# Kernel tuning notes

Hardware: AMD Instinct MI355X
Metric: run time of the kernel (lower is better)

The kernel has to match this reference:

```python
import jax, jax.numpy as jnp
import numpy as np

NEG_SLOPE = 0.2  # PyG GATv2Conv default
TOPK = 10        # hard-coded in original forward


def setup_inputs() -> dict:
    key = jax.random.key(0)
    N, E, D, L = 50000, 640000, 128, 3
    ks = jax.random.split(key, 12)
    s = 1.0 / np.sqrt(D)
    x = jax.random.normal(ks[0], (N, D), jnp.float32)
    edge_index = jax.random.randint(ks[1], (2, E), 0, N, dtype=jnp.int64)
    edge_attributes = jax.random.normal(ks[2], (E, D), jnp.float32)
    # GATv2 per-layer params (heads=1): lin_l (src), lin_r (dst), lin_edge, att, out bias
    Wl = jax.random.normal(ks[3], (L, D, D), jnp.float32) * s
    bl = jnp.zeros((L, D), jnp.float32)
    Wr = jax.random.normal(ks[4], (L, D, D), jnp.float32) * s
    br = jnp.zeros((L, D), jnp.float32)
    We = jax.random.normal(ks[5], (L, D, D), jnp.float32) * s
    att = jax.random.normal(ks[6], (L, D), jnp.float32) * s
    bias = jnp.zeros((L, D), jnp.float32)
    # final Conv1d(D, 1, 1) == linear projection D -> 1 per node
    Wf = jax.random.normal(ks[7], (D, 1), jnp.float32) * s
    bf = jnp.zeros((1,), jnp.float32)
    return {"x": x, "edge_index": edge_index, "edge_attributes": edge_attributes,
            "Wl": Wl, "bl": bl, "Wr": Wr, "br": br, "We": We, "att": att,
            "bias": bias, "Wf": Wf, "bf": bf}


def _gatv2_layer(x, src, dst, ea, N, Wl, bl, Wr, br, We, att, bias):
    xl = x @ Wl + bl            # [N, D] source transform
    xr = x @ Wr + br            # [N, D] target transform
    ee = ea @ We                # [E', D] edge transform (no bias in PyG lin_edge)
    m = jax.nn.leaky_relu(xl[src] + xr[dst] + ee, NEG_SLOPE)  # [E', D]
    logits = m @ att            # [E']
    # per-destination softmax (every node has a self-loop -> no empty segments)
    mx = jax.ops.segment_max(logits, dst, num_segments=N)
    w = jnp.exp(logits - mx[dst])
    den = jax.ops.segment_sum(w, dst, num_segments=N)
    alpha = w / den[dst]
    out = jax.ops.segment_sum(xl[src] * alpha[:, None], dst, num_segments=N)
    return out + bias


def reference(x, edge_index, edge_attributes, Wl, bl, Wr, br, We, att, bias, Wf, bf):
    N, D = x.shape
    src, dst = edge_index[0], edge_index[1]
    loop = jnp.arange(N, dtype=src.dtype)
    # add_self_loops with fill_value='mean': loop attr = mean of incoming edge attrs
    cnt = jax.ops.segment_sum(jnp.ones_like(dst, dtype=x.dtype), dst, num_segments=N)
    loop_attr = jax.ops.segment_sum(edge_attributes, dst, num_segments=N) / jnp.maximum(cnt, 1.0)[:, None]
    src_f = jnp.concatenate([src, loop])
    dst_f = jnp.concatenate([dst, loop])
    ea = jnp.concatenate([edge_attributes, loop_attr], axis=0)
    L = Wl.shape[0]
    for i in range(L):
        x = _gatv2_layer(x, src_f, dst_f, ea, N, Wl[i], bl[i], Wr[i], br[i], We[i], att[i], bias[i])
    scores = (x @ Wf)[:, 0] + bf[0]   # Conv1d(D,1,1): per-node scalar score [N]
    vals, idx = jax.lax.top_k(scores, TOPK)
    return vals, idx
```

## Files before the change

### kernel.cpp

```cpp
#include <hip/hip_runtime.h>
#include <hip/hip_bf16.h>
#include <float.h>

#define DD 128
#define NEG_SLOPE 0.2f

typedef __attribute__((ext_vector_type(8))) short bf16x8;
typedef __attribute__((ext_vector_type(4))) float f32x4;

__device__ __forceinline__ float lrelu(float v) {
    return fmaxf(v, 0.0f) + NEG_SLOPE * fminf(v, 0.0f);
}

__device__ __forceinline__ unsigned short f2bf(float f) {
    unsigned u = __float_as_uint(f);
    u += 0x7fff + ((u >> 16) & 1);
    return (unsigned short)(u >> 16);
}
__device__ __forceinline__ float bf2f(unsigned short h) {
    return __uint_as_float(((unsigned)h) << 16);
}


__global__ void k_hist(const int* __restrict__ dst, int E, int* __restrict__ cnt) {
    int i = blockIdx.x * blockDim.x + threadIdx.x;
    if (i < E) atomicAdd(&cnt[dst[i]], 1);
}

__global__ __launch_bounds__(1024) void k_scan(const int* __restrict__ cnt,
                                               int* __restrict__ row_ptr, int N) {
    __shared__ int sums[1024];
    int tid = threadIdx.x;
    int total = N + 1;
    int chunk = (total + 1023) / 1024;
    int lo = tid * chunk;
    int hi = min(lo + chunk, total);
    int s = 0;
    for (int i = lo; i < hi; ++i) s += (i < N) ? (cnt[i] + 1) : 0;
    sums[tid] = s;
    __syncthreads();
    for (int off = 1; off < 1024; off <<= 1) {
        int t = (tid >= off) ? sums[tid - off] : 0;
        __syncthreads();
        sums[tid] += t;
        __syncthreads();
    }
    int run = sums[tid] - s;
    for (int i = lo; i < hi; ++i) {
        row_ptr[i] = run;
        run += (i < N) ? (cnt[i] + 1) : 0;
    }
}

__global__ void k_scatter(const int* __restrict__ dst, int E, int N,
                          const int* __restrict__ row_ptr, int* __restrict__ fill,
                          const int* __restrict__ cnt, int* __restrict__ eids) {
    int i = blockIdx.x * blockDim.x + threadIdx.x;
    int tot = E + N;
    if (i >= tot) return;
    if (i < E) {
        int d = dst[i];
        int p = atomicAdd(&fill[d], 1);
        eids[row_ptr[d] + p] = i;
    } else {
        int n = i - E;
        eids[row_ptr[n] + cnt[n]] = E + n;
    }
}

__global__ void k_sort_rows(const int* __restrict__ row_ptr, int* __restrict__ eids, int N) {
    int n = blockIdx.x * blockDim.x + threadIdx.x;
    if (n >= N) return;
    int s = row_ptr[n], e = row_ptr[n + 1];
    for (int i = s + 1; i < e; ++i) {
        int v = eids[i];
        int j = i - 1;
        while (j >= s && eids[j] > v) { eids[j + 1] = eids[j]; --j; }
        eids[j + 1] = v;
    }
}

__global__ void k_invert(const int* __restrict__ eids, const int* __restrict__ srcArr,
                         int* __restrict__ pos, int* __restrict__ csr_src, int Etot, int E) {
    int p = blockIdx.x * blockDim.x + threadIdx.x;
    if (p >= Etot) return;
    int eid = eids[p];
    pos[eid] = p;
    csr_src[p] = (eid < E) ? srcArr[eid] : (eid - E);
}

__global__ __launch_bounds__(256) void k_loop_attr(const float* __restrict__ ea,
                                                   const int* __restrict__ row_ptr,
                                                   const int* __restrict__ cnt,
                                                   const int* __restrict__ eids,
                                                   float* __restrict__ loop_attr, int N) {
    int wid = (blockIdx.x * blockDim.x + threadIdx.x) >> 6;
    int lane = threadIdx.x & 63;
    if (wid >= N) return;
    int s = row_ptr[wid];
    int c = cnt[wid];
    float2 acc = make_float2(0.f, 0.f);
    for (int c0 = 0; c0 < c; c0 += 64) {
        int m = min(64, c - c0);
        int eid = 0;
        if (lane < m) eid = eids[s + c0 + lane];
        int p = 0;
        for (; p + 4 <= m; p += 4) {
            int e0 = __shfl(eid, p), e1 = __shfl(eid, p + 1);
            int e2 = __shfl(eid, p + 2), e3 = __shfl(eid, p + 3);
            float2 v0 = *reinterpret_cast<const float2*>(ea + (size_t)e0 * DD + 2 * lane);
            float2 v1 = *reinterpret_cast<const float2*>(ea + (size_t)e1 * DD + 2 * lane);
            float2 v2 = *reinterpret_cast<const float2*>(ea + (size_t)e2 * DD + 2 * lane);
            float2 v3 = *reinterpret_cast<const float2*>(ea + (size_t)e3 * DD + 2 * lane);
            acc.x += v0.x; acc.y += v0.y;
            acc.x += v1.x; acc.y += v1.y;
            acc.x += v2.x; acc.y += v2.y;
            acc.x += v3.x; acc.y += v3.y;
        }
        for (; p < m; ++p) {
            int e = __shfl(eid, p);
            float2 v = *reinterpret_cast<const float2*>(ea + (size_t)e * DD + 2 * lane);
            acc.x += v.x; acc.y += v.y;
        }
    }
    float inv = 1.0f / fmaxf((float)c, 1.0f);
    float2 o = make_float2(acc.x * inv, acc.y * inv);
    *reinterpret_cast<float2*>(loop_attr + (size_t)wid * DD + 2 * lane) = o;
}

__global__ void k_prepack(const float* __restrict__ W, unsigned short* __restrict__ WA, int L) {
    int idx = blockIdx.x * blockDim.x + threadIdx.x;
    int total = L * DD * DD;
    if (idx >= total) return;
    int l = idx >> 14;
    int rem = idx & 16383;
    int k = rem >> 7;
    int j = rem & 127;
    float w = W[(size_t)l * 16384 + (size_t)k * DD + j];
    unsigned short h = f2bf(w);
    unsigned short lo = f2bf(w - bf2f(h));
    int ks = k >> 5, g = (k >> 3) & 3, i = k & 7;
    size_t off = ((size_t)(ks * 4 + g) * DD + j) * 8 + i;
    unsigned short* base = WA + (size_t)l * 32768;
    base[off] = h;
    base[16384 + off] = lo;
}


__global__ __launch_bounds__(512, 2) void k_gemm_mfma(
    const float* __restrict__ X, const unsigned short* __restrict__ WA,
    const float* __restrict__ b, float* __restrict__ Y, int N) {

    __shared__ unsigned short WAs[32768];
    {
        const uint4* gsrc = reinterpret_cast<const uint4*>(WA);
        uint4* ldst = reinterpret_cast<uint4*>(WAs);
        int t = threadIdx.x;
        #pragma unroll
        for (int i = 0; i < 8; ++i) ldst[t + i * 512] = gsrc[t + i * 512];
    }
    __syncthreads();

    int tid  = threadIdx.x;
    int lane = tid & 63;
    int wv   = tid >> 6;
    int lc   = lane & 15;
    int g    = lane >> 4;

    int r0 = blockIdx.x * 256 + wv * 32;
    int rv[2]; bool ok[2];
    const float* rp[2];
    #pragma unroll
    for (int nf = 0; nf < 2; ++nf) {
        rv[nf] = r0 + nf * 16 + lc;
        ok[nf] = (rv[nf] < N);
        rp[nf] = X + (size_t)(ok[nf] ? rv[nf] : 0) * DD;
    }

    f32x4 acc[8][2];
    #pragma unroll
    for (int m = 0; m < 8; ++m)
        #pragma unroll
        for (int n = 0; n < 2; ++n)
            acc[m][n] = (f32x4){0.f, 0.f, 0.f, 0.f};

    float4 pr0[2], pr1[2];
    #pragma unroll
    for (int nf = 0; nf < 2; ++nf) {
        pr0[nf] = *reinterpret_cast<const float4*>(rp[nf] + g * 8);
        pr1[nf] = *reinterpret_cast<const float4*>(rp[nf] + g * 8 + 4);
    }

    #pragma unroll
    for (int ks = 0; ks < 4; ++ks) {
        bf16x8 Bh[2], Bl[2];
        #pragma unroll
        for (int nf = 0; nf < 2; ++nf) {
            float v[8] = {pr0[nf].x, pr0[nf].y, pr0[nf].z, pr0[nf].w,
                          pr1[nf].x, pr1[nf].y, pr1[nf].z, pr1[nf].w};
            #pragma unroll
            for (int i = 0; i < 8; ++i) {
                unsigned short h = f2bf(v[i]);
                Bh[nf][i] = (short)h;
                Bl[nf][i] = (short)f2bf(v[i] - bf2f(h));
            }
        }
        if (ks < 3) {
            int k0n = (ks + 1) * 32 + g * 8;
            #pragma unroll
            for (int nf = 0; nf < 2; ++nf) {
                pr0[nf] = *reinterpret_cast<const float4*>(rp[nf] + k0n);
                pr1[nf] = *reinterpret_cast<const float4*>(rp[nf] + k0n + 4);
            }
        }
        #pragma unroll
        for (int mf = 0; mf < 8; ++mf) {
            int aoff = ((ks * 4 + g) * DD + (mf * 16 + lc)) * 8;
            bf16x8 Ah = *reinterpret_cast<const bf16x8*>(&WAs[aoff]);
            bf16x8 Al = *reinterpret_cast<const bf16x8*>(&WAs[16384 + aoff]);
            #pragma unroll
            for (int nf = 0; nf < 2; ++nf) {
                acc[mf][nf] = __builtin_amdgcn_mfma_f32_16x16x32_bf16(Ah, Bh[nf], acc[mf][nf], 0, 0, 0);
                acc[mf][nf] = __builtin_amdgcn_mfma_f32_16x16x32_bf16(Al, Bh[nf], acc[mf][nf], 0, 0, 0);
                acc[mf][nf] = __builtin_amdgcn_mfma_f32_16x16x32_bf16(Ah, Bl[nf], acc[mf][nf], 0, 0, 0);
            }
        }
    }

    #pragma unroll
    for (int mf = 0; mf < 8; ++mf) {
        int f0 = mf * 16 + g * 4;
        float4 bv = *reinterpret_cast<const float4*>(b + f0);
        #pragma unroll
        for (int nf = 0; nf < 2; ++nf) {
            if (!ok[nf]) continue;
            float4 o;
            o.x = acc[mf][nf][0] + bv.x;
            o.y = acc[mf][nf][1] + bv.y;
            o.z = acc[mf][nf][2] + bv.z;
            o.w = acc[mf][nf][3] + bv.w;
            *reinterpret_cast<float4*>(Y + (size_t)rv[nf] * DD + f0) = o;
        }
    }
}

__global__ __launch_bounds__(512, 2) void k_edge_mfma(
    const float* __restrict__ ea, const float* __restrict__ loop_attr,
    const int* __restrict__ srcArr, const int* __restrict__ dstArr,
    const unsigned short* __restrict__ WA, const float* __restrict__ att,
    const float* __restrict__ xl, const float* __restrict__ xr,
    const int* __restrict__ pos, float* __restrict__ wlog, int E, int Etot) {

    __shared__ unsigned short WAs[32768];
    {
        const uint4* gsrc = reinterpret_cast<const uint4*>(WA);
        uint4* ldst = reinterpret_cast<uint4*>(WAs);
        int t = threadIdx.x;
        #pragma unroll
        for (int i = 0; i < 8; ++i) ldst[t + i * 512] = gsrc[t + i * 512];
    }
    __syncthreads();

    int tid  = threadIdx.x;
    int lane = tid & 63;
    int wv   = tid >> 6;
    int lc   = lane & 15;
    int g    = lane >> 4;

    int e0 = blockIdx.x * 256 + wv * 32;

    const float* rp[2];
    int ev[2]; bool ok[2];
    #pragma unroll
    for (int nf = 0; nf < 2; ++nf) {
        int e = e0 + nf * 16 + lc;
        ev[nf] = e;
        ok[nf] = (e < Etot);
        if (e < E)         rp[nf] = ea + (size_t)e * DD;
        else if (e < Etot) rp[nf] = loop_attr + (size_t)(e - E) * DD;
        else               rp[nf] = ea;
    }

    f32x4 acc[8][2];
    #pragma unroll
    for (int m = 0; m < 8; ++m)
        #pragma unroll
        for (int n = 0; n < 2; ++n)
            acc[m][n] = (f32x4){0.f, 0.f, 0.f, 0.f};

    float4 pr0[2], pr1[2];
    #pragma unroll
    for (int nf = 0; nf < 2; ++nf) {
        pr0[nf] = *reinterpret_cast<const float4*>(rp[nf] + g * 8);
        pr1[nf] = *reinterpret_cast<const float4*>(rp[nf] + g * 8 + 4);
    }

    #pragma unroll
    for (int ks = 0; ks < 4; ++ks) {
        bf16x8 Bh[2], Bl[2];
        #pragma unroll
        for (int nf = 0; nf < 2; ++nf) {
            float v[8] = {pr0[nf].x, pr0[nf].y, pr0[nf].z, pr0[nf].w,
                          pr1[nf].x, pr1[nf].y, pr1[nf].z, pr1[nf].w};
            #pragma unroll
            for (int i = 0; i < 8; ++i) {
                unsigned short h = f2bf(v[i]);
                Bh[nf][i] = (short)h;
                Bl[nf][i] = (short)f2bf(v[i] - bf2f(h));
            }
        }
        if (ks < 3) {
            int k0n = (ks + 1) * 32 + g * 8;
            #pragma unroll
            for (int nf = 0; nf < 2; ++nf) {
                pr0[nf] = *reinterpret_cast<const float4*>(rp[nf] + k0n);
                pr1[nf] = *reinterpret_cast<const float4*>(rp[nf] + k0n + 4);
            }
        }
        #pragma unroll
        for (int mf = 0; mf < 8; ++mf) {
            int aoff = ((ks * 4 + g) * DD + (mf * 16 + lc)) * 8;
            bf16x8 Ah = *reinterpret_cast<const bf16x8*>(&WAs[aoff]);
            bf16x8 Al = *reinterpret_cast<const bf16x8*>(&WAs[16384 + aoff]);
            #pragma unroll
            for (int nf = 0; nf < 2; ++nf) {
                acc[mf][nf] = __builtin_amdgcn_mfma_f32_16x16x32_bf16(Ah, Bh[nf], acc[mf][nf], 0, 0, 0);
                acc[mf][nf] = __builtin_amdgcn_mfma_f32_16x16x32_bf16(Al, Bh[nf], acc[mf][nf], 0, 0, 0);
                acc[mf][nf] = __builtin_amdgcn_mfma_f32_16x16x32_bf16(Ah, Bl[nf], acc[mf][nf], 0, 0, 0);
            }
        }
    }

    int sn[2], dn[2];
    #pragma unroll
    for (int nf = 0; nf < 2; ++nf) {
        int e = ev[nf];
        if (e < E)       { sn[nf] = srcArr[e]; dn[nf] = dstArr[e]; }
        else if (ok[nf]) { sn[nf] = e - E; dn[nf] = e - E; }
        else             { sn[nf] = 0; dn[nf] = 0; }
    }
    float partial[2] = {0.f, 0.f};
    #pragma unroll
    for (int mf = 0; mf < 8; ++mf) {
        int f0 = mf * 16 + g * 4;
        float4 attv = *reinterpret_cast<const float4*>(att + f0);
        #pragma unroll
        for (int nf = 0; nf < 2; ++nf) {
            float4 xlv = *reinterpret_cast<const float4*>(xl + (size_t)sn[nf] * DD + f0);
            float4 xrv = *reinterpret_cast<const float4*>(xr + (size_t)dn[nf] * DD + f0);
            float t0 = acc[mf][nf][0] + xlv.x + xrv.x;
            float t1 = acc[mf][nf][1] + xlv.y + xrv.y;
            float t2 = acc[mf][nf][2] + xlv.z + xrv.z;
            float t3 = acc[mf][nf][3] + xlv.w + xrv.w;
            partial[nf] += attv.x * lrelu(t0) + attv.y * lrelu(t1)
                         + attv.z * lrelu(t2) + attv.w * lrelu(t3);
        }
    }
    #pragma unroll
    for (int nf = 0; nf < 2; ++nf) {
        float p = partial[nf];
        p += __shfl_xor(p, 16);
        p += __shfl_xor(p, 32);
        if (lane < 16 && ok[nf]) wlog[pos[ev[nf]]] = p;
    }
}

__global__ __launch_bounds__(256) void k_sfx_agg(
    const float* __restrict__ wlog, const int* __restrict__ row_ptr,
    const int* __restrict__ csr_src, const float* __restrict__ xl,
    const float* __restrict__ bias, float* __restrict__ xout, int N) {
    int wid = (blockIdx.x * blockDim.x + threadIdx.x) >> 6;
    int lane = threadIdx.x & 63;
    if (wid >= N) return;
    int s = row_ptr[wid], e = row_ptr[wid + 1];
    float mx = -FLT_MAX;
    for (int c0 = s; c0 < e; c0 += 64) {
        float l = (c0 + lane < e) ? wlog[c0 + lane] : -FLT_MAX;
        l = fmaxf(l, __shfl_xor(l, 32));
        l = fmaxf(l, __shfl_xor(l, 16));
        l = fmaxf(l, __shfl_xor(l, 8));
        l = fmaxf(l, __shfl_xor(l, 4));
        l = fmaxf(l, __shfl_xor(l, 2));
        l = fmaxf(l, __shfl_xor(l, 1));
        mx = fmaxf(mx, l);
    }
    float den = 0.f;
    for (int c0 = s; c0 < e; c0 += 64) {
        float w = (c0 + lane < e) ? __expf(wlog[c0 + lane] - mx) : 0.f;
        w += __shfl_xor(w, 32);
        w += __shfl_xor(w, 16);
        w += __shfl_xor(w, 8);
        w += __shfl_xor(w, 4);
        w += __shfl_xor(w, 2);
        w += __shfl_xor(w, 1);
        den += w;
    }
    float inv = 1.0f / den;
    float2 acc = make_float2(0.f, 0.f);
    for (int c0 = s; c0 < e; c0 += 64) {
        int m = min(64, e - c0);
        float av = 0.f; int sv = 0;
        if (lane < m) {
            av = __expf(wlog[c0 + lane] - mx) * inv;
            sv = csr_src[c0 + lane];
        }
        int p = 0;
        for (; p + 4 <= m; p += 4) {
            float a0 = __shfl(av, p),     a1 = __shfl(av, p + 1);
            float a2 = __shfl(av, p + 2), a3 = __shfl(av, p + 3);
            int   r0 = __shfl(sv, p),     r1 = __shfl(sv, p + 1);
            int   r2 = __shfl(sv, p + 2), r3 = __shfl(sv, p + 3);
            float2 v0 = *reinterpret_cast<const float2*>(xl + (size_t)r0 * DD + 2 * lane);
            float2 v1 = *reinterpret_cast<const float2*>(xl + (size_t)r1 * DD + 2 * lane);
            float2 v2 = *reinterpret_cast<const float2*>(xl + (size_t)r2 * DD + 2 * lane);
            float2 v3 = *reinterpret_cast<const float2*>(xl + (size_t)r3 * DD + 2 * lane);
            acc.x += a0 * v0.x; acc.y += a0 * v0.y;
            acc.x += a1 * v1.x; acc.y += a1 * v1.y;
            acc.x += a2 * v2.x; acc.y += a2 * v2.y;
            acc.x += a3 * v3.x; acc.y += a3 * v3.y;
        }
        for (; p < m; ++p) {
            float ap = __shfl(av, p);
            int   rw = __shfl(sv, p);
            float2 v = *reinterpret_cast<const float2*>(xl + (size_t)rw * DD + 2 * lane);
            acc.x += ap * v.x;
            acc.y += ap * v.y;
        }
    }
    float2 bv = *reinterpret_cast<const float2*>(bias + 2 * lane);
    float2 o = make_float2(acc.x + bv.x, acc.y + bv.y);
    *reinterpret_cast<float2*>(xout + (size_t)wid * DD + 2 * lane) = o;
}


__global__ __launch_bounds__(256) void k_scores(const float* __restrict__ X,
                                                const float* __restrict__ Wf,
                                                const float* __restrict__ bf,
                                                float* __restrict__ scores, int N) {
    int gid = blockIdx.x * blockDim.x + threadIdx.x;
    int node = gid >> 6;
    int lane = threadIdx.x & 63;
    if (node >= N) return;
    float2 xv = *reinterpret_cast<const float2*>(&X[(size_t)node * DD + lane * 2]);
    float2 wv = *reinterpret_cast<const float2*>(&Wf[lane * 2]);
    float p = xv.x * wv.x + xv.y * wv.y;
    p += __shfl_xor(p, 32);
    p += __shfl_xor(p, 16);
    p += __shfl_xor(p, 8);
    p += __shfl_xor(p, 4);
    p += __shfl_xor(p, 2);
    p += __shfl_xor(p, 1);
    if (lane == 0) scores[node] = p + bf[0];
}

__device__ __forceinline__ bool tk_better(float a, int ai, float b, int bi) {
    return (a > b) || (a == b && ai < bi);
}

__global__ __launch_bounds__(1024) void k_topk(const float* __restrict__ scores, int N,
                                               float* __restrict__ out) {
    __shared__ float lv[1024 * 10];
    __shared__ int li[1024 * 10];
    int t = threadIdx.x;
    float v[10]; int ix[10];
    #pragma unroll
    for (int j = 0; j < 10; ++j) { v[j] = -FLT_MAX; ix[j] = 0x7fffffff; }
    for (int i = t; i < N; i += 1024) {
        float sv = scores[i];
        if (tk_better(sv, i, v[9], ix[9])) {
            v[9] = sv; ix[9] = i;
            #pragma unroll
            for (int j = 9; j > 0; --j) {
                if (tk_better(v[j], ix[j], v[j - 1], ix[j - 1])) {
                    float tv = v[j]; v[j] = v[j - 1]; v[j - 1] = tv;
                    int ti = ix[j]; ix[j] = ix[j - 1]; ix[j - 1] = ti;
                }
            }
        }
    }
    #pragma unroll
    for (int j = 0; j < 10; ++j) { lv[t * 10 + j] = v[j]; li[t * 10 + j] = ix[j]; }
    __syncthreads();
    for (int sh = 512; sh >= 1; sh >>= 1) {
        if (t < sh) {
            float bv[10]; int bi[10];
            #pragma unroll
            for (int j = 0; j < 10; ++j) { bv[j] = lv[(t + sh) * 10 + j]; bi[j] = li[(t + sh) * 10 + j]; }
            float mv[10]; int mi[10];
            int i1 = 0, i2 = 0;
            #pragma unroll
            for (int k = 0; k < 10; ++k) {
                if (tk_better(v[i1], ix[i1], bv[i2], bi[i2])) { mv[k] = v[i1]; mi[k] = ix[i1]; ++i1; }
                else { mv[k] = bv[i2]; mi[k] = bi[i2]; ++i2; }
            }
            #pragma unroll
            for (int j = 0; j < 10; ++j) {
                v[j] = mv[j]; ix[j] = mi[j];
                lv[t * 10 + j] = v[j]; li[t * 10 + j] = ix[j];
            }
        }
        __syncthreads();
    }
    if (t == 0) {
        #pragma unroll
        for (int j = 0; j < 10; ++j) {
            out[j] = v[j];
            out[10 + j] = (float)ix[j];
        }
    }
}


static inline size_t alignup(size_t v) { return (v + 255) & ~(size_t)255; }

extern "C" void kernel_launch(void* const* d_in, const int* in_sizes, int n_in,
                              void* d_out, int out_size, void* d_ws, size_t ws_size,
                              hipStream_t stream) {
    const float* x    = (const float*)d_in[0];
    const int*   ei   = (const int*)d_in[1];
    const float* ea   = (const float*)d_in[2];
    const float* Wl   = (const float*)d_in[3];
    const float* bl   = (const float*)d_in[4];
    const float* Wr   = (const float*)d_in[5];
    const float* br   = (const float*)d_in[6];
    const float* We   = (const float*)d_in[7];
    const float* att  = (const float*)d_in[8];
    const float* bias = (const float*)d_in[9];
    const float* Wf   = (const float*)d_in[10];
    const float* bf   = (const float*)d_in[11];

    int N = in_sizes[0] / DD;
    int E = in_sizes[1] / 2;
    int L = in_sizes[3] / (DD * DD);
    int Etot = E + N;
    const int* src = ei;
    const int* dst = ei + E;

    size_t off = 0;
    char* wsb = (char*)d_ws;
    auto carve = [&](size_t bytes) -> void* { void* p = wsb + off; off += alignup(bytes); return p; };
    unsigned short* WAe = (unsigned short*)carve((size_t)L * 32768 * 2);
    unsigned short* WAl = (unsigned short*)carve((size_t)L * 32768 * 2);
    unsigned short* WAr = (unsigned short*)carve((size_t)L * 32768 * 2);
    int*   cnt       = (int*)carve((size_t)N * 4);
    int*   fill      = (int*)carve((size_t)N * 4);
    int*   row_ptr   = (int*)carve((size_t)(N + 1) * 4);
    int*   eids      = (int*)carve((size_t)Etot * 4);
    int*   pos       = (int*)carve((size_t)Etot * 4);
    int*   csr_src   = (int*)carve((size_t)Etot * 4);
    float* wlog      = (float*)carve((size_t)Etot * 4);
    float* loop_attr = (float*)carve((size_t)N * DD * 4);
    float* xl        = (float*)carve((size_t)N * DD * 4);
    float* xr        = (float*)carve((size_t)N * DD * 4);
    float* xa        = (float*)carve((size_t)N * DD * 4);
    float* xb        = (float*)carve((size_t)N * DD * 4);
    float* scoresBuf = (float*)carve((size_t)N * 4);
    (void)ws_size; (void)n_in; (void)out_size;

    hipMemsetAsync(cnt, 0, (size_t)N * 4, stream);
    hipMemsetAsync(fill, 0, (size_t)N * 4, stream);

    int ppBlocks = (L * DD * DD + 255) / 256;
    k_prepack<<<ppBlocks, 256, 0, stream>>>(We, WAe, L);
    k_prepack<<<ppBlocks, 256, 0, stream>>>(Wl, WAl, L);
    k_prepack<<<ppBlocks, 256, 0, stream>>>(Wr, WAr, L);
    k_hist<<<(E + 255) / 256, 256, 0, stream>>>(dst, E, cnt);
    k_scan<<<1, 1024, 0, stream>>>(cnt, row_ptr, N);
    k_scatter<<<(Etot + 255) / 256, 256, 0, stream>>>(dst, E, N, row_ptr, fill, cnt, eids);
    k_sort_rows<<<(N + 255) / 256, 256, 0, stream>>>(row_ptr, eids, N);
    k_invert<<<(Etot + 255) / 256, 256, 0, stream>>>(eids, src, pos, csr_src, Etot, E);
    int waveBlocks = (N * 64 + 255) / 256;
    k_loop_attr<<<waveBlocks, 256, 0, stream>>>(ea, row_ptr, cnt, eids, loop_attr, N);

    const float* xin = x;
    float* xout = xa;
    int gemmBlocks = (N + 255) / 256;
    int edgeBlocks = (Etot + 255) / 256;
    for (int l = 0; l < L; ++l) {
        k_gemm_mfma<<<gemmBlocks, 512, 0, stream>>>(xin, WAl + (size_t)l * 32768, bl + (size_t)l * DD, xl, N);
        k_gemm_mfma<<<gemmBlocks, 512, 0, stream>>>(xin, WAr + (size_t)l * 32768, br + (size_t)l * DD, xr, N);
        k_edge_mfma<<<edgeBlocks, 512, 0, stream>>>(ea, loop_attr, src, dst,
                                                    WAe + (size_t)l * 32768, att + (size_t)l * DD,
                                                    xl, xr, pos, wlog, E, Etot);
        k_sfx_agg<<<waveBlocks, 256, 0, stream>>>(wlog, row_ptr, csr_src, xl,
                                                  bias + (size_t)l * DD, xout, N);
        xin = xout;
        xout = (xout == xa) ? xb : xa;
    }
    k_scores<<<(N + 3) / 4, 256, 0, stream>>>(xin, Wf, bf, scoresBuf, N);
    k_topk<<<1, 1024, 0, stream>>>(scoresBuf, N, (float*)d_out);
}
```

Baseline: 1.205 ms.

## Split top-k into multi-block candidate pass and single-block final merge

Replaces the single 1024-thread top-k kernel with a two-stage reduction: 128 blocks each compute a local top-10 over a strided slice of scores, then a 64-thread kernel merges the 1280 candidates. This spreads the scan of the 50k scores over many compute units instead of one, and shortens the shared-memory merge tree. It adds one kernel launch and a small candidate buffer.

Result: no change. 1.221 ms (median of 2 runs) (+1.4%).

```diff
diff --git a/kernel.cpp b/kernel.cpp
--- a/kernel.cpp
+++ b/kernel.cpp
@@ -4,6 +4,7 @@
 
 #define DD 128
 #define NEG_SLOPE 0.2f
+#define TKB 128
 
 typedef __attribute__((ext_vector_type(8))) short bf16x8;
 typedef __attribute__((ext_vector_type(4))) float f32x4;
@@ -457,31 +458,76 @@
     return (a > b) || (a == b && ai < bi);
 }
 
-__global__ __launch_bounds__(1024) void k_topk(const float* __restrict__ scores, int N,
-                                               float* __restrict__ out) {
-    __shared__ float lv[1024 * 10];
-    __shared__ int li[1024 * 10];
+__device__ __forceinline__ void tk_insert(float sv, int si, float* v, int* ix) {
+    if (tk_better(sv, si, v[9], ix[9])) {
+        v[9] = sv; ix[9] = si;
+        #pragma unroll
+        for (int j = 9; j > 0; --j) {
+            if (tk_better(v[j], ix[j], v[j - 1], ix[j - 1])) {
+                float tv = v[j]; v[j] = v[j - 1]; v[j - 1] = tv;
+                int ti = ix[j]; ix[j] = ix[j - 1]; ix[j - 1] = ti;
+            }
+        }
+    }
+}
+
+__global__ __launch_bounds__(256) void k_topk1(const float* __restrict__ scores, int N,
+                                               float* __restrict__ cand_v, int* __restrict__ cand_i) {
+    __shared__ float lv[256 * 10];
+    __shared__ int li[256 * 10];
     int t = threadIdx.x;
     float v[10]; int ix[10];
     #pragma unroll
     for (int j = 0; j < 10; ++j) { v[j] = -FLT_MAX; ix[j] = 0x7fffffff; }
-    for (int i = t; i < N; i += 1024) {
-        float sv = scores[i];
-        if (tk_better(sv, i, v[9], ix[9])) {
-            v[9] = sv; ix[9] = i;
-            #pragma unroll
-            for (int j = 9; j > 0; --j) {
-                if (tk_better(v[j], ix[j], v[j - 1], ix[j - 1])) {
-                    float tv = v[j]; v[j] = v[j - 1]; v[j - 1] = tv;
-                    int ti = ix[j]; ix[j] = ix[j - 1]; ix[j - 1] = ti;
-                }
-            }
-        }
-    }
+    for (int i = blockIdx.x * 256 + t; i < N; i += TKB * 256)
+        tk_insert(scores[i], i, v, ix);
     #pragma unroll
     for (int j = 0; j < 10; ++j) { lv[t * 10 + j] = v[j]; li[t * 10 + j] = ix[j]; }
     __syncthreads();
-    for (int sh = 512; sh >= 1; sh >>= 1) {
+    for (int sh = 128; sh >= 1; sh >>= 1) {
+        if (t < sh) {
+            float bv[10]; int bi[10];
+            #pragma unroll
+            for (int j = 0; j < 10; ++j) { bv[j] = lv[(t + sh) * 10 + j]; bi[j] = li[(t + sh) * 10 + j]; }
+            float mv[10]; int mi[10];
+            int i1 = 0, i2 = 0;
+            #pragma unroll
+            for (int k = 0; k < 10; ++k) {
+                if (tk_better(v[i1], ix[i1], bv[i2], bi[i2])) { mv[k] = v[i1]; mi[k] = ix[i1]; ++i1; }
+                else { mv[k] = bv[i2]; mi[k] = bi[i2]; ++i2; }
+            }
+            #pragma unroll
+            for (int j = 0; j < 10; ++j) {
+                v[j] = mv[j]; ix[j] = mi[j];
+                lv[t * 10 + j] = v[j]; li[t * 10 + j] = ix[j];
+            }
+        }
+        __syncthreads();
+    }
+    if (t == 0) {
+        #pragma unroll
+        for (int j = 0; j < 10; ++j) {
+            cand_v[blockIdx.x * 10 + j] = v[j];
+            cand_i[blockIdx.x * 10 + j] = ix[j];
+        }
+    }
+}
+
+__global__ __launch_bounds__(64) void k_topk2(const float* __restrict__ cand_v,
+                                              const int* __restrict__ cand_i,
+                                              float* __restrict__ out) {
+    __shared__ float lv[64 * 10];
+    __shared__ int li[64 * 10];
+    int t = threadIdx.x;
+    float v[10]; int ix[10];
+    #pragma unroll
+    for (int j = 0; j < 10; ++j) { v[j] = -FLT_MAX; ix[j] = 0x7fffffff; }
+    for (int i = t; i < TKB * 10; i += 64)
+        tk_insert(cand_v[i], cand_i[i], v, ix);
+    #pragma unroll
+    for (int j = 0; j < 10; ++j) { lv[t * 10 + j] = v[j]; li[t * 10 + j] = ix[j]; }
+    __syncthreads();
+    for (int sh = 32; sh >= 1; sh >>= 1) {
         if (t < sh) {
             float bv[10]; int bi[10];
             #pragma unroll
@@ -555,6 +601,8 @@
     float* xa        = (float*)carve((size_t)N * DD * 4);
     float* xb        = (float*)carve((size_t)N * DD * 4);
     float* scoresBuf = (float*)carve((size_t)N * 4);
+    float* cand_v    = (float*)carve((size_t)TKB * 10 * 4);
+    int*   cand_i    = (int*)carve((size_t)TKB * 10 * 4);
     (void)ws_size; (void)n_in; (void)out_size;
 
     hipMemsetAsync(cnt, 0, (size_t)N * 4, stream);
@@ -588,5 +636,6 @@
         xout = (xout == xa) ? xb : xa;
     }
     k_scores<<<(N + 3) / 4, 256, 0, stream>>>(xin, Wf, bf, scoresBuf, N);
-    k_topk<<<1, 1024, 0, stream>>>(scoresBuf, N, (float*)d_out);
-}
+    k_topk1<<<TKB, 256, 0, stream>>>(scoresBuf, N, cand_v, cand_i);
+    k_topk2<<<1, 64, 0, stream>>>(cand_v, cand_i, (float*)d_out);
+}
```
